# Kernel optimization log

Measured on AMD Instinct MI355X. Metric: run time of the kernel, lower is better.

## Reference

```python
import jax, jax.numpy as jnp
import numpy as np

B, NF, NB, E = 32768, 64, 33, 64  # batch, num_features, boundaries per feature, embedding size


def setup_inputs() -> dict:
    key = jax.random.key(0)
    kx, kb, kw = jax.random.split(key, 3)
    X = jax.random.normal(kx, (B, NF), dtype=jnp.float32)
    # strictly increasing per-feature boundaries: cumsum of positive steps
    steps = jax.random.uniform(kb, (NF, NB), dtype=jnp.float32, minval=0.05, maxval=0.2)
    bounds = jnp.cumsum(steps, axis=1) - 2.0  # roughly centered around the data range
    W = jax.random.normal(kw, (NF, NB - 1, E), dtype=jnp.float32) / np.sqrt(NB - 1).astype(np.float32)
    b = jnp.zeros((NF, E), dtype=jnp.float32)
    return {"X": X, "bounds": bounds, "W": W, "b": b}


def reference(X, bounds, W, b):
    # Piecewise-linear bin encoding, vectorized over all features at once.
    lo = bounds[:, :-1]            # [NF, NB-1]
    hi = bounds[:, 1:]             # [NF, NB-1]
    scale = hi - lo                # [NF, NB-1]
    x = X[:, :, None]              # [B, NF, 1]
    enc = (jax.nn.relu(x - lo[None]) - jax.nn.relu(x - hi[None])) / scale  # [B, NF, NB-1]
    # Per-feature Linear + ReLU (block-diagonal / grouped GEMM), then concat over features
    out = jax.nn.relu(jnp.einsum('bfi,fie->bfe', enc, W) + b[None])       # [B, NF, E]
    return out.reshape(X.shape[0], -1)                                     # [B, NF*E]
```

## Files before the change

kernel.cpp:

```cpp
#include <hip/hip_runtime.h>

#define B_TOT 32768
#define NF    64
#define NB    33
#define NSEG  32
#define E     64
#define BPB   256

__global__ __launch_bounds__(256) void pwl_kernel(
    const float* __restrict__ X,
    const float* __restrict__ bounds,
    const float* __restrict__ W,
    const float* __restrict__ bias,
    float* __restrict__ out)
{
    __shared__ __align__(16) float sW[NSEG][E];
    __shared__ __align__(16) float sP[NB][E];
    __shared__ float sBounds[NB];
    __shared__ float sFrac[BPB];
    __shared__ int   sJ[BPB];

    const int f   = blockIdx.x;
    const int tid = threadIdx.x;
    const int b0  = blockIdx.y * BPB;

    {
        const float4* Wg  = reinterpret_cast<const float4*>(W + f * (NSEG * E));
        float4*       sW4 = reinterpret_cast<float4*>(&sW[0][0]);
        sW4[tid]       = Wg[tid];
        sW4[tid + 256] = Wg[tid + 256];
        if (tid < NB) sBounds[tid] = bounds[f * NB + tid];
    }
    __syncthreads();

    if (tid < E) {
        float acc = bias[f * E + tid];
        sP[0][tid] = acc;
        #pragma unroll
        for (int i = 0; i < NSEG; ++i) {
            acc += sW[i][tid];
            sP[i + 1][tid] = acc;
        }
    }
    __syncthreads();

    {
        const float x = X[(b0 + tid) * NF + f];
        int c = 0;
        #pragma unroll
        for (int i = 0; i < NB; ++i) c += (sBounds[i] <= x) ? 1 : 0;
        int j = c - 1;
        j = (j < 0) ? 0 : ((j > NSEG - 1) ? NSEG - 1 : j);
        const float lo = sBounds[j];
        const float hi = sBounds[j + 1];
        float fr = (x - lo) / (hi - lo);
        fr = fminf(fmaxf(fr, 0.0f), 1.0f);
        sJ[tid]   = j;
        sFrac[tid] = fr;
    }
    __syncthreads();

    const int q = tid & 15;
    const int g = tid >> 4;
    const float4* sP4 = reinterpret_cast<const float4*>(&sP[0][0]);
    const float4* sW4 = reinterpret_cast<const float4*>(&sW[0][0]);
    float4* out4 = reinterpret_cast<float4*>(out);
    const int colbase = f * (E / 4) + q;

    #pragma unroll 4
    for (int k = 0; k < 16; ++k) {
        const int idx = k * 16 + g;
        const int   j  = sJ[idx];
        const float fr = sFrac[idx];
        const float4 p = sP4[j * 16 + q];
        const float4 w = sW4[j * 16 + q];
        float4 r;
        r.x = fmaxf(fmaf(fr, w.x, p.x), 0.0f);
        r.y = fmaxf(fmaf(fr, w.y, p.y), 0.0f);
        r.z = fmaxf(fmaf(fr, w.z, p.z), 0.0f);
        r.w = fmaxf(fmaf(fr, w.w, p.w), 0.0f);
        out4[(b0 + idx) * (NF * E / 4) + colbase] = r;
    }
}

extern "C" void kernel_launch(void* const* d_in, const int* in_sizes, int n_in,
                              void* d_out, int out_size, void* d_ws, size_t ws_size,
                              hipStream_t stream) {
    const float* X      = (const float*)d_in[0];
    const float* bounds = (const float*)d_in[1];
    const float* W      = (const float*)d_in[2];
    const float* bias   = (const float*)d_in[3];
    float* out          = (float*)d_out;

    dim3 grid(NF, B_TOT / BPB);
    dim3 block(256);
    pwl_kernel<<<grid, block, 0, stream>>>(X, bounds, W, bias, out);
}
```

Measured before the change: 538.4 us.

## Interleave prefix sums and weights in shared memory, restructure output stores per wavefront

Packs the prefix-sum table and the weights into one interleaved float4 shared array, so each output pair needs a single LDS read. Bin index and fraction are packed into one uint2. The X load is hoisted ahead of the weight copy, and the prefix computation now overlaps the bin search, which removes one barrier. Each wavefront now writes two rows at a time as float2 stores, instead of float4 stores across 16 rows per block. The aim is fewer LDS transactions and syncs, at the cost of narrower global stores.

```diff
diff --git a/kernel.cpp b/kernel.cpp
--- a/kernel.cpp
+++ b/kernel.cpp
@@ -14,38 +14,32 @@
     const float* __restrict__ bias,
     float* __restrict__ out)
 {
-    __shared__ __align__(16) float sW[NSEG][E];
-    __shared__ __align__(16) float sP[NB][E];
+    __shared__ __align__(16) float4 sPW[NSEG][E / 2];
     __shared__ float sBounds[NB];
-    __shared__ float sFrac[BPB];
-    __shared__ int   sJ[BPB];
+    __shared__ uint2 sJF[BPB];
 
     const int f   = blockIdx.x;
     const int tid = threadIdx.x;
     const int b0  = blockIdx.y * BPB;
 
+    const float x = X[(size_t)(b0 + tid) * NF + f];
+    float biasv = 0.0f;
+    if (tid < E) biasv = bias[f * E + tid];
+
     {
-        const float4* Wg  = reinterpret_cast<const float4*>(W + f * (NSEG * E));
-        float4*       sW4 = reinterpret_cast<float4*>(&sW[0][0]);
-        sW4[tid]       = Wg[tid];
-        sW4[tid + 256] = Wg[tid + 256];
+        const float2* Wg  = reinterpret_cast<const float2*>(W + f * (NSEG * E));
+        float*        flat = &sPW[0][0].x;
+        #pragma unroll
+        for (int t = 0; t < 4; ++t) {
+            const int idx = tid + t * 256;
+            const float2 w2 = Wg[idx];
+            *reinterpret_cast<float2*>(flat + idx * 4 + 2) = w2;
+        }
         if (tid < NB) sBounds[tid] = bounds[f * NB + tid];
     }
     __syncthreads();
 
-    if (tid < E) {
-        float acc = bias[f * E + tid];
-        sP[0][tid] = acc;
-        #pragma unroll
-        for (int i = 0; i < NSEG; ++i) {
-            acc += sW[i][tid];
-            sP[i + 1][tid] = acc;
-        }
-    }
-    __syncthreads();
-
     {
-        const float x = X[(b0 + tid) * NF + f];
         int c = 0;
         #pragma unroll
         for (int i = 0; i < NB; ++i) c += (sBounds[i] <= x) ? 1 : 0;
@@ -55,31 +49,45 @@
         const float hi = sBounds[j + 1];
         float fr = (x - lo) / (hi - lo);
         fr = fminf(fmaxf(fr, 0.0f), 1.0f);
-        sJ[tid]   = j;
-        sFrac[tid] = fr;
+        sJF[tid] = make_uint2((unsigned)j, __float_as_uint(fr));
+    }
+
+    if (tid < E) {
+        const int e2 = tid >> 1;
+        const int c  = tid & 1;
+        float acc = biasv;
+        float* flat = &sPW[0][0].x;
+        #pragma unroll
+        for (int i = 0; i < NSEG; ++i) {
+            float* cell = flat + (i * 32 + e2) * 4;
+            const float w = cell[2 + c];
+            cell[c] = acc;
+            acc += w;
+        }
     }
     __syncthreads();
 
-    const int q = tid & 15;
-    const int g = tid >> 4;
-    const float4* sP4 = reinterpret_cast<const float4*>(&sP[0][0]);
-    const float4* sW4 = reinterpret_cast<const float4*>(&sW[0][0]);
-    float4* out4 = reinterpret_cast<float4*>(out);
-    const int colbase = f * (E / 4) + q;
+    const int lane  = tid & 63;
+    const int wv    = tid >> 6;
+    const int half  = lane >> 5;
+    const int e2    = lane & 31;
+    const int wbase = wv * 64;
 
-    #pragma unroll 4
-    for (int k = 0; k < 16; ++k) {
-        const int idx = k * 16 + g;
-        const int   j  = sJ[idx];
-        const float fr = sFrac[idx];
-        const float4 p = sP4[j * 16 + q];
-        const float4 w = sW4[j * 16 + q];
-        float4 r;
-        r.x = fmaxf(fmaf(fr, w.x, p.x), 0.0f);
-        r.y = fmaxf(fmaf(fr, w.y, p.y), 0.0f);
-        r.z = fmaxf(fmaf(fr, w.z, p.z), 0.0f);
-        r.w = fmaxf(fmaf(fr, w.w, p.w), 0.0f);
-        out4[(b0 + idx) * (NF * E / 4) + colbase] = r;
+    const float4* __restrict__ PW = &sPW[0][0];
+    float2* outp = reinterpret_cast<float2*>(
+        out + (size_t)(b0 + wbase + half) * (NF * E) + f * E + 2 * e2);
+
+    #pragma unroll 8
+    for (int it = 0; it < 32; ++it) {
+        const uint2 jf = sJF[wbase + 2 * it + half];
+        const int   j  = (int)jf.x;
+        const float fr = __uint_as_float(jf.y);
+        const float4 v = PW[j * 32 + e2];
+        float2 r;
+        r.x = fmaxf(fmaf(fr, v.z, v.x), 0.0f);
+        r.y = fmaxf(fmaf(fr, v.w, v.y), 0.0f);
+        *outp = r;
+        outp += 4096;
     }
 }
 
```

Result: no change. 539.4 us (+0.2%).
